# Optimization experiments

Hardware: AMD Instinct MI355X
Metric: run time of the kernel (lower is better)

The kernel has to match this reference:

```python
import jax, jax.numpy as jnp
import numpy as np

FEATURE_DIM = 68
ONE_HOT_MAX = 29  # one-hot coordinate features only for coords < 29


def _compute_encodings(height, width):
    # height, width are static Python ints
    xs = jnp.arange(width, dtype=jnp.float32)
    ys = jnp.arange(height, dtype=jnp.float32)

    def axis_feats(coords, size):
        if size > 1:
            norm = 2.0 * (coords / (size - 1)) - 1.0
            angle = jnp.pi * (coords / (size - 1))
        else:
            norm = jnp.zeros_like(coords)
            angle = jnp.zeros_like(coords)
        sign = jnp.sign(coords - size / 2.0)  # -1 / 0 / +1 around midpoint
        rtan = jnp.round(jnp.tan(angle))
        return jnp.stack([norm, sign, jnp.sin(angle), jnp.cos(angle), rtan], axis=-1)  # [size, 5]

    xf = axis_feats(xs, width)    # [W, 5] -> feature slots 0,2,4,6,8
    yf = axis_feats(ys, height)   # [H, 5] -> feature slots 1,3,5,7,9

    xb = jnp.broadcast_to(xf[None, :, :], (height, width, 5))
    yb = jnp.broadcast_to(yf[:, None, :], (height, width, 5))
    # interleave x/y features -> order x0,y0,x1,y1,... matches slots 0..9
    first10 = jnp.stack([xb, yb], axis=-1).reshape(height, width, 10)

    idx = jnp.arange(ONE_HOT_MAX)
    ohx = (xs[:, None] == idx[None, :]).astype(jnp.float32)  # [W, 29], zero rows for x >= 29
    ohy = (ys[:, None] == idx[None, :]).astype(jnp.float32)  # [H, 29]
    ohx_b = jnp.broadcast_to(ohx[None, :, :], (height, width, ONE_HOT_MAX))
    ohy_b = jnp.broadcast_to(ohy[:, None, :], (height, width, ONE_HOT_MAX))

    return jnp.concatenate([first10, ohx_b, ohy_b], axis=-1)  # [H, W, 68]


def setup_inputs() -> dict:
    key = jax.random.key(0)
    H, W, B = 512, 512, 8
    x = jax.random.normal(key, (B, H * W), dtype=jnp.float32)
    return {"x": x, "height": H, "width": W}


def reference(x, height, width):
    batch_size, seq_len = x.shape
    enc = _compute_encodings(height, width).reshape(-1, FEATURE_DIM)  # [H*W, 68]
    enc_b = jnp.broadcast_to(enc[None, :, :], (batch_size, seq_len, FEATURE_DIM))
    return jnp.concatenate([x[..., None], enc_b], axis=-1)  # [B, H*W, 69]
```

## Files before the change

kernel.cpp:

```cpp
#include <hip/hip_runtime.h>
#include <math.h>

typedef float f32x4 __attribute__((ext_vector_type(4)));

#define NF 69u
#define WROWS 64u
#define WTILE_FLOATS (WROWS * NF)
#define WTILE_F4 (WTILE_FLOATS / 4u)
#define NCHUNK 18u
#define BLOCK 256u
#define WAVES 4u

__global__ void pe_table_kernel(const int* __restrict__ hptr,
                                const int* __restrict__ wptr,
                                float* __restrict__ tab8) {
    const int H = *hptr;
    const int W = *wptr;
    const int total = W + H;
    for (int i = (int)(blockIdx.x * blockDim.x + threadIdx.x); i < total;
         i += (int)(gridDim.x * blockDim.x)) {
        const bool is_y = (i >= W);
        const int c = is_y ? (i - W) : i;
        const int size = is_y ? H : W;
        double norm = 0.0, angle = 0.0;
        if (size > 1) {
            const double r = (double)c / (double)(size - 1);
            norm = 2.0 * r - 1.0;
            angle = M_PI * r;
        }
        const double d = (double)c - 0.5 * (double)size;
        const float sgn = (d > 0.0) ? 1.0f : ((d < 0.0) ? -1.0f : 0.0f);
        const int base = (is_y ? 8 * W : 0) + 8 * c;
        tab8[base + 0] = (float)norm;
        tab8[base + 1] = sgn;
        tab8[base + 2] = (float)sin(angle);
        tab8[base + 3] = (float)cos(angle);
        tab8[base + 4] = (float)rint(tan(angle));
    }
}

__global__ __launch_bounds__(BLOCK) void pe_main_kernel(
    const float* __restrict__ x,
    const int* __restrict__ hptr, const int* __restrict__ wptr,
    const float* __restrict__ tab8,
    float* __restrict__ out, unsigned int Q ) {
    __shared__ __align__(16) float lds[WAVES][WTILE_FLOATS];

    const unsigned int W = (unsigned int)*wptr;
    const unsigned int H = (unsigned int)*hptr;
    const unsigned int yoff8 = 8u * W;
    const unsigned int lane = threadIdx.x & 63u;
    const unsigned int wid = threadIdx.x >> 6;
    float* buf = lds[wid];

    {
        f32x4 z = {0.f, 0.f, 0.f, 0.f};
        f32x4* bp = (f32x4*)buf;
        for (unsigned int j = lane; j < WTILE_F4; j += 64u) bp[j] = z;
    }

    const unsigned int ntiles = (Q + WROWS - 1u) / WROWS;
    const unsigned int gw = blockIdx.x * WAVES + wid;
    const unsigned int nw = gridDim.x * WAVES;

    for (unsigned int T = gw; T < ntiles; T += nw) {
        const unsigned int q = T * WROWS + lane;
        unsigned int w = 0u, h = 0u;
        const bool valid = q < Q;
        if (valid) {
            const unsigned int t = q / W;
            w = q - t * W;
            h = t - (t / H) * H;
            float* row = buf + lane * NF;
            row[0] = x[q];
            const f32x4 xa = *(const f32x4*)(tab8 + 8u * w);
            const float xa4 = tab8[8u * w + 4u];
            const f32x4 ya = *(const f32x4*)(tab8 + yoff8 + 8u * h);
            const float ya4 = tab8[yoff8 + 8u * h + 4u];
            row[1] = xa[0]; row[2]  = ya[0];
            row[3] = xa[1]; row[4]  = ya[1];
            row[5] = xa[2]; row[6]  = ya[2];
            row[7] = xa[3]; row[8]  = ya[3];
            row[9] = xa4;   row[10] = ya4;
            if (w < 29u) row[11u + w] = 1.0f;
            if (h < 29u) row[40u + h] = 1.0f;
        }

        const unsigned int rem = Q - T * WROWS;
        const size_t obase = (size_t)T * (size_t)WTILE_FLOATS;
        const f32x4* lp = (const f32x4*)buf;
        f32x4* op = (f32x4*)(out + obase);

        if (rem >= WROWS) {
            f32x4 v[NCHUNK];
#pragma unroll
            for (unsigned int j = 0u; j < NCHUNK; ++j) {
                const unsigned int idx = lane + 64u * j;
                if (j < NCHUNK - 1u || idx < WTILE_F4) v[j] = lp[idx];
            }
#pragma unroll
            for (unsigned int j = 0u; j < NCHUNK; ++j) {
                const unsigned int idx = lane + 64u * j;
                if (j < NCHUNK - 1u || idx < WTILE_F4)
                    __builtin_nontemporal_store(v[j], op + idx);
            }
        } else {
            const unsigned int nfl = rem * NF;
            const unsigned int n4 = nfl >> 2;
            for (unsigned int j = lane; j < n4; j += 64u)
                __builtin_nontemporal_store(lp[j], op + j);
            for (unsigned int j = (n4 << 2) + lane; j < nfl; j += 64u)
                __builtin_nontemporal_store(buf[j], out + obase + j);
        }

        if (valid) {
            float* row = buf + lane * NF;
            if (w < 29u) row[11u + w] = 0.0f;
            if (h < 29u) row[40u + h] = 0.0f;
        }
    }
}

extern "C" void kernel_launch(void* const* d_in, const int* in_sizes, int n_in,
                              void* d_out, int out_size, void* d_ws, size_t ws_size,
                              hipStream_t stream) {
    const float* x = (const float*)d_in[0];
    const int* hptr = (const int*)d_in[1];
    const int* wptr = (const int*)d_in[2];
    float* out = (float*)d_out;
    float* tab8 = (float*)d_ws;

    pe_table_kernel<<<8, 256, 0, stream>>>(hptr, wptr, tab8);

    const unsigned int Q = (unsigned int)in_sizes[0];
    const unsigned int ntiles = (Q + WROWS - 1u) / WROWS;
    unsigned int blocks = (ntiles + WAVES - 1u) / WAVES;
    if (blocks > 2048u) blocks = 2048u;
    if (blocks == 0u) blocks = 1u;
    pe_main_kernel<<<blocks, BLOCK, 0, stream>>>(x, hptr, wptr, tab8, out, Q);
}
```

Measured before the change: 118.4 us.

## Share 64-row tiles across block with double-buffered LDS and split fill work

Each block now cooperatively handles one 64-row tile at a time instead of each wave owning its own tile. Filling the tile is divided among the four waves by column group, and the fill is double-buffered in LDS so the next tile is built while the current one is streamed out. A power-of-two shortcut replaces the integer divisions used for the w/h index math. The exchange is one block-wide barrier per tile and more LDS bookkeeping, since one-hot clears now track the previous index per buffer.

```diff
diff --git a/kernel.cpp b/kernel.cpp
--- a/kernel.cpp
+++ b/kernel.cpp
@@ -4,12 +4,10 @@
 typedef float f32x4 __attribute__((ext_vector_type(4)));
 
 #define NF 69u
-#define WROWS 64u
-#define WTILE_FLOATS (WROWS * NF)
-#define WTILE_F4 (WTILE_FLOATS / 4u)
-#define NCHUNK 18u
+#define TROWS 64u
+#define TILE_FLOATS (TROWS * NF)
+#define TILE_F4 (TILE_FLOATS / 4u)
 #define BLOCK 256u
-#define WAVES 4u
 
 __global__ void pe_table_kernel(const int* __restrict__ hptr,
                                 const int* __restrict__ wptr,
@@ -39,85 +37,121 @@
     }
 }
 
+__device__ __forceinline__ void pe_compute(
+    float* __restrict__ buf, unsigned int T, unsigned int Q,
+    unsigned int W, unsigned int H, unsigned int yoff8,
+    bool pot, unsigned int lw,
+    const float* __restrict__ x, const float* __restrict__ tab8,
+    unsigned int lane, unsigned int wv,
+    unsigned int& pw, unsigned int& ph) {
+    const unsigned int q = T * TROWS + lane;
+    const bool valid = q < Q;
+    unsigned int w, h;
+    if (pot) {
+        w = q & (W - 1u);
+        h = (q >> lw) & (H - 1u);
+    } else {
+        const unsigned int t = q / W;
+        w = q - t * W;
+        h = t - (t / H) * H;
+    }
+    float* row = buf + lane * NF;
+    const float* tx = tab8 + 8u * w;
+    const float* ty = tab8 + yoff8 + 8u * h;
+    if (wv == 0u) {
+        if (valid) { row[0] = x[q]; row[1] = tx[0]; row[2] = ty[0]; }
+    } else if (wv == 1u) {
+        if (valid) { row[3] = tx[1]; row[4] = ty[1]; row[5] = tx[2]; }
+    } else if (wv == 2u) {
+        if (valid) { row[6] = ty[2]; row[7] = tx[3]; }
+        if (pw < 29u) row[11u + pw] = 0.0f;
+        const unsigned int npw = (valid && w < 29u) ? w : 0xFFFFFFFFu;
+        if (npw < 29u) row[11u + npw] = 1.0f;
+        pw = npw;
+    } else {
+        if (valid) { row[8] = ty[3]; row[9] = tx[4]; row[10] = ty[4]; }
+        if (ph < 29u) row[40u + ph] = 0.0f;
+        const unsigned int nph = (valid && h < 29u) ? h : 0xFFFFFFFFu;
+        if (nph < 29u) row[40u + nph] = 1.0f;
+        ph = nph;
+    }
+}
+
 __global__ __launch_bounds__(BLOCK) void pe_main_kernel(
     const float* __restrict__ x,
     const int* __restrict__ hptr, const int* __restrict__ wptr,
     const float* __restrict__ tab8,
     float* __restrict__ out, unsigned int Q ) {
-    __shared__ __align__(16) float lds[WAVES][WTILE_FLOATS];
+    __shared__ __align__(16) float lds[2][TILE_FLOATS];
 
     const unsigned int W = (unsigned int)*wptr;
     const unsigned int H = (unsigned int)*hptr;
     const unsigned int yoff8 = 8u * W;
+    const bool pot = ((W & (W - 1u)) == 0u) && ((H & (H - 1u)) == 0u);
+    const unsigned int lw = pot ? (unsigned int)(__ffs((int)W) - 1) : 0u;
     const unsigned int lane = threadIdx.x & 63u;
-    const unsigned int wid = threadIdx.x >> 6;
-    float* buf = lds[wid];
+    const unsigned int wv = threadIdx.x >> 6;
+    const unsigned int ntiles = (Q + TROWS - 1u) / TROWS;
+    const unsigned int g = gridDim.x;
 
     {
         f32x4 z = {0.f, 0.f, 0.f, 0.f};
-        f32x4* bp = (f32x4*)buf;
-        for (unsigned int j = lane; j < WTILE_F4; j += 64u) bp[j] = z;
+        f32x4* bp = (f32x4*)&lds[0][0];
+        for (unsigned int j = threadIdx.x; j < 2u * TILE_F4; j += BLOCK)
+            bp[j] = z;
     }
+    __syncthreads();
 
-    const unsigned int ntiles = (Q + WROWS - 1u) / WROWS;
-    const unsigned int gw = blockIdx.x * WAVES + wid;
-    const unsigned int nw = gridDim.x * WAVES;
+    unsigned int T = blockIdx.x;
+    if (T >= ntiles) return;
 
-    for (unsigned int T = gw; T < ntiles; T += nw) {
-        const unsigned int q = T * WROWS + lane;
-        unsigned int w = 0u, h = 0u;
-        const bool valid = q < Q;
-        if (valid) {
-            const unsigned int t = q / W;
-            w = q - t * W;
-            h = t - (t / H) * H;
-            float* row = buf + lane * NF;
-            row[0] = x[q];
-            const f32x4 xa = *(const f32x4*)(tab8 + 8u * w);
-            const float xa4 = tab8[8u * w + 4u];
-            const f32x4 ya = *(const f32x4*)(tab8 + yoff8 + 8u * h);
-            const float ya4 = tab8[yoff8 + 8u * h + 4u];
-            row[1] = xa[0]; row[2]  = ya[0];
-            row[3] = xa[1]; row[4]  = ya[1];
-            row[5] = xa[2]; row[6]  = ya[2];
-            row[7] = xa[3]; row[8]  = ya[3];
-            row[9] = xa4;   row[10] = ya4;
-            if (w < 29u) row[11u + w] = 1.0f;
-            if (h < 29u) row[40u + h] = 1.0f;
-        }
+    unsigned int pw0 = 0xFFFFFFFFu, ph0 = 0xFFFFFFFFu;
+    unsigned int pw1 = 0xFFFFFFFFu, ph1 = 0xFFFFFFFFu;
+    pe_compute(lds[0], T, Q, W, H, yoff8, pot, lw, x, tab8, lane, wv, pw0, ph0);
+    unsigned int cur = 0u;
 
-        const unsigned int rem = Q - T * WROWS;
-        const size_t obase = (size_t)T * (size_t)WTILE_FLOATS;
-        const f32x4* lp = (const f32x4*)buf;
+    for (; T < ntiles; T += g) {
+        asm volatile("s_waitcnt lgkmcnt(0)\n\ts_barrier" ::: "memory");
+
+        const unsigned int rem = Q - T * TROWS;
+        const size_t obase = (size_t)T * (size_t)TILE_FLOATS;
+        const f32x4* lp = (const f32x4*)(cur ? lds[1] : lds[0]);
         f32x4* op = (f32x4*)(out + obase);
 
-        if (rem >= WROWS) {
-            f32x4 v[NCHUNK];
-#pragma unroll
-            for (unsigned int j = 0u; j < NCHUNK; ++j) {
-                const unsigned int idx = lane + 64u * j;
-                if (j < NCHUNK - 1u || idx < WTILE_F4) v[j] = lp[idx];
-            }
-#pragma unroll
-            for (unsigned int j = 0u; j < NCHUNK; ++j) {
-                const unsigned int idx = lane + 64u * j;
-                if (j < NCHUNK - 1u || idx < WTILE_F4)
-                    __builtin_nontemporal_store(v[j], op + idx);
-            }
+        if (rem >= TROWS) {
+            const unsigned int t0 = threadIdx.x;
+            const bool m = t0 < (TILE_F4 - 4u * BLOCK);
+            f32x4 v0 = lp[t0];
+            f32x4 v1 = lp[t0 + 256u];
+            f32x4 v2 = lp[t0 + 512u];
+            f32x4 v3 = lp[t0 + 768u];
+            f32x4 v4;
+            if (m) v4 = lp[t0 + 1024u];
+            __builtin_nontemporal_store(v0, op + t0);
+            __builtin_nontemporal_store(v1, op + t0 + 256u);
+            __builtin_nontemporal_store(v2, op + t0 + 512u);
+            __builtin_nontemporal_store(v3, op + t0 + 768u);
+            if (m) __builtin_nontemporal_store(v4, op + t0 + 1024u);
         } else {
             const unsigned int nfl = rem * NF;
             const unsigned int n4 = nfl >> 2;
-            for (unsigned int j = lane; j < n4; j += 64u)
+            const float* lf = (const float*)lp;
+            for (unsigned int j = threadIdx.x; j < n4; j += BLOCK)
                 __builtin_nontemporal_store(lp[j], op + j);
-            for (unsigned int j = (n4 << 2) + lane; j < nfl; j += 64u)
-                __builtin_nontemporal_store(buf[j], out + obase + j);
+            for (unsigned int j = (n4 << 2) + threadIdx.x; j < nfl; j += BLOCK)
+                __builtin_nontemporal_store(lf[j], out + obase + j);
         }
 
-        if (valid) {
-            float* row = buf + lane * NF;
-            if (w < 29u) row[11u + w] = 0.0f;
-            if (h < 29u) row[40u + h] = 0.0f;
+        const unsigned int Tn = T + g;
+        if (Tn < ntiles) {
+            if (cur == 0u)
+                pe_compute(lds[1], Tn, Q, W, H, yoff8, pot, lw, x, tab8,
+                           lane, wv, pw1, ph1);
+            else
+                pe_compute(lds[0], Tn, Q, W, H, yoff8, pot, lw, x, tab8,
+                           lane, wv, pw0, ph0);
         }
+        cur ^= 1u;
     }
 }
 
@@ -133,9 +167,8 @@
     pe_table_kernel<<<8, 256, 0, stream>>>(hptr, wptr, tab8);
 
     const unsigned int Q = (unsigned int)in_sizes[0];
-    const unsigned int ntiles = (Q + WROWS - 1u) / WROWS;
-    unsigned int blocks = (ntiles + WAVES - 1u) / WAVES;
-    if (blocks > 2048u) blocks = 2048u;
+    const unsigned int ntiles = (Q + TROWS - 1u) / TROWS;
+    unsigned int blocks = ntiles < 2048u ? ntiles : 2048u;
     if (blocks == 0u) blocks = 1u;
     pe_main_kernel<<<blocks, BLOCK, 0, stream>>>(x, hptr, wptr, tab8, out, Q);
 }
```

Result: no change. 119.7 us (+1.1%).
